# Kernel optimization log

Hardware: AMD Instinct MI355X
Metric: run time of the kernel (lower is better)

## Reference

```python
import jax, jax.numpy as jnp
import numpy as np

N_ATOMS = 3
HIDDEN = 256
N_PAIRS = N_ATOMS * (N_ATOMS - 1) // 2  # 3
BATCH = 500000


def setup_inputs() -> dict:
    key = jax.random.key(0)
    ks = jax.random.split(key, 8)
    s1 = 1.0 / np.sqrt(N_PAIRS)
    s2 = 1.0 / np.sqrt(HIDDEN)
    return {
        "x": jax.random.normal(ks[0], (BATCH, N_ATOMS * 3), dtype=jnp.float32),
        "W1": jax.random.normal(ks[1], (N_PAIRS, HIDDEN), dtype=jnp.float32) * s1,
        "b1": jnp.zeros((HIDDEN,), dtype=jnp.float32),
        "W2": jax.random.normal(ks[2], (HIDDEN, HIDDEN), dtype=jnp.float32) * s2,
        "b2": jnp.zeros((HIDDEN,), dtype=jnp.float32),
        "W3": jax.random.normal(ks[3], (HIDDEN, 3), dtype=jnp.float32) * s2,
        "b3": jnp.zeros((3,), dtype=jnp.float32),
    }


def reference(x, W1, b1, W2, b2, W3, b3):
    # --- pairwise bond lengths (vectorized over batch) ---
    pts = x.reshape(-1, N_ATOMS, 3)                       # [B, n_atoms, 3]
    iu, ju = np.triu_indices(N_ATOMS, 1)                  # static index arrays
    diff = pts[:, iu, :] - pts[:, ju, :]                  # [B, n_pairs, 3]
    r = jnp.sqrt(jnp.sum(diff * diff, axis=-1))           # [B, n_pairs]
    # --- MLP: Dense->relu->Dense->relu->Dense (sizes=[256,256,3]) ---
    h = jax.nn.relu(r @ W1 + b1)                          # [B, 256]
    h = jax.nn.relu(h @ W2 + b2)                          # [B, 256]
    w = h @ W3 + b3                                       # [B, 3] -> (w00, w11, w01)
    # --- analytic eigenvalues of symmetric 2x2 [[w00,w01],[w01,w11]] ---
    # eigh returns ascending order: mean -/+ radius
    m = 0.5 * (w[:, 0] + w[:, 1])
    d = 0.5 * (w[:, 0] - w[:, 1])
    rad = jnp.sqrt(d * d + w[:, 2] * w[:, 2])
    return jnp.stack([m - rad, m + rad], axis=-1)         # [B, 2]
```

## Files before the change

### kernel.cpp

```cpp
#include <hip/hip_runtime.h>
#include <hip/hip_bf16.h>
#include <stdint.h>

typedef __attribute__((ext_vector_type(8))) short short8;
typedef __attribute__((ext_vector_type(4))) float f32x4;

#define NCHUNK 15625
#define NBLK 256
#define NTHR 512
#define NWAVE_TOT (NBLK * 8)

__device__ __forceinline__ unsigned short f2bf(float f) {
    unsigned int u = __float_as_uint(f);
    u = (u + 0x7fffu + ((u >> 16) & 1u)) >> 16;
    return (unsigned short)u;
}

__global__ void prep_kernel(const float* __restrict__ W1, const float* __restrict__ b1,
                            const float* __restrict__ W2, const float* __restrict__ b2,
                            const float* __restrict__ W3,
                            uint4* __restrict__ w2p, float4* __restrict__ w1b1,
                            float4* __restrict__ w3b2) {
    int id = blockIdx.x * 256 + threadIdx.x;
    if (id < 8192) {
        int lane = id & 63;
        int f = id >> 6;
        int s = f >> 4, t = f & 15;
        int g = lane >> 4, c = lane & 15;
        int n = t * 16 + c;
        int kbase = s * 32 + g * 8;
        unsigned int w[4];
#pragma unroll
        for (int jj = 0; jj < 4; ++jj) {
            unsigned int lo = f2bf(W2[(kbase + 2 * jj) * 256 + n]);
            unsigned int hi = f2bf(W2[(kbase + 2 * jj + 1) * 256 + n]);
            w[jj] = lo | (hi << 16);
        }
        w2p[id] = make_uint4(w[0], w[1], w[2], w[3]);
    } else if (id < 8448) {
        int k = id - 8192;
        w1b1[k] = make_float4(W1[k], W1[256 + k], W1[512 + k], b1[k]);
    } else if (id < 8704) {
        int c2 = id - 8448;
        w3b2[c2] = make_float4(W3[c2 * 3 + 0], W3[c2 * 3 + 1], W3[c2 * 3 + 2], b2[c2]);
    }
}

__global__ __launch_bounds__(NTHR, 2) void fused_kernel(
    const float* __restrict__ x, const uint4* __restrict__ w2p,
    const float4* __restrict__ w1b1, const float4* __restrict__ w3b2,
    const float* __restrict__ b3, float* __restrict__ out)
{
    extern __shared__ char smem[];
    const int tid = threadIdx.x;
    const int lane = tid & 63;
    const int g = lane >> 4;
    const int lr = lane & 15;

    {
        uint4* ls = (uint4*)smem;
#pragma unroll
        for (int it = 0; it < 16; ++it) {
            int idx = it * NTHR + tid;
            ls[idx] = w2p[idx];
        }
    }
    __syncthreads();

    const float b30 = b3[0], b31 = b3[1], b32 = b3[2];
    const short8* bfr = (const short8*)smem;
    const int gwave = blockIdx.x * 8 + (tid >> 6);

    for (int chunk = gwave; chunk < NCHUNK; chunk += NWAVE_TOT) {
        const int row0 = chunk * 32;

        float q0[2], q1[2], q2[2];
#pragma unroll
        for (int mt = 0; mt < 2; ++mt) {
            const float* xp = x + (long)(row0 + mt * 16 + lr) * 9;
            float d0 = xp[0] - xp[3], d1 = xp[1] - xp[4], d2 = xp[2] - xp[5];
            float e0 = xp[0] - xp[6], e1 = xp[1] - xp[7], e2 = xp[2] - xp[8];
            float f0 = xp[3] - xp[6], f1 = xp[4] - xp[7], f2 = xp[5] - xp[8];
            q0[mt] = sqrtf(d0 * d0 + d1 * d1 + d2 * d2);
            q1[mt] = sqrtf(e0 * e0 + e1 * e1 + e2 * e2);
            q2[mt] = sqrtf(f0 * f0 + f1 * f1 + f2 * f2);
        }

        f32x4 acc[2][16];
        const f32x4 zz = {0.0f, 0.0f, 0.0f, 0.0f};
#pragma unroll
        for (int t = 0; t < 16; ++t) { acc[0][t] = zz; acc[1][t] = zz; }

#pragma unroll 1
        for (int s = 0; s < 8; ++s) {
            short8 a0v, a1v;
#pragma unroll
            for (int j = 0; j < 8; ++j) {
                float4 wb = w1b1[s * 32 + g * 8 + j];
                float h0 = fmaf(q0[0], wb.x, fmaf(q1[0], wb.y, fmaf(q2[0], wb.z, wb.w)));
                float h1 = fmaf(q0[1], wb.x, fmaf(q1[1], wb.y, fmaf(q2[1], wb.z, wb.w)));
                a0v[j] = (short)f2bf(fmaxf(h0, 0.0f));
                a1v[j] = (short)f2bf(fmaxf(h1, 0.0f));
            }
#pragma unroll
            for (int t = 0; t < 16; ++t) {
                short8 bv = bfr[(s * 16 + t) * 64 + lane];
                acc[0][t] = __builtin_amdgcn_mfma_f32_16x16x32_bf16(a0v, bv, acc[0][t], 0, 0, 0);
                acc[1][t] = __builtin_amdgcn_mfma_f32_16x16x32_bf16(a1v, bv, acc[1][t], 0, 0, 0);
            }
        }

        float p[2][4][3];
#pragma unroll
        for (int mt = 0; mt < 2; ++mt)
#pragma unroll
            for (int r = 0; r < 4; ++r) { p[mt][r][0] = 0.f; p[mt][r][1] = 0.f; p[mt][r][2] = 0.f; }

#pragma unroll
        for (int t = 0; t < 16; ++t) {
            float4 wb = w3b2[t * 16 + lr];
#pragma unroll
            for (int mt = 0; mt < 2; ++mt)
#pragma unroll
                for (int r = 0; r < 4; ++r) {
                    float v = fmaxf(acc[mt][t][r] + wb.w, 0.0f);
                    p[mt][r][0] = fmaf(v, wb.x, p[mt][r][0]);
                    p[mt][r][1] = fmaf(v, wb.y, p[mt][r][1]);
                    p[mt][r][2] = fmaf(v, wb.z, p[mt][r][2]);
                }
        }

#pragma unroll
        for (int mt = 0; mt < 2; ++mt)
#pragma unroll
            for (int r = 0; r < 4; ++r)
#pragma unroll
                for (int m = 0; m < 3; ++m) {
                    float v = p[mt][r][m];
                    v += __shfl_xor(v, 1, 16);
                    v += __shfl_xor(v, 2, 16);
                    v += __shfl_xor(v, 4, 16);
                    v += __shfl_xor(v, 8, 16);
                    p[mt][r][m] = v;
                }

        if (lr == 0) {
#pragma unroll
            for (int mt = 0; mt < 2; ++mt)
#pragma unroll
                for (int r = 0; r < 4; ++r) {
                    float w0 = p[mt][r][0] + b30;
                    float w1v = p[mt][r][1] + b31;
                    float w2v = p[mt][r][2] + b32;
                    float mm = 0.5f * (w0 + w1v);
                    float dd = 0.5f * (w0 - w1v);
                    float rad = sqrtf(fmaf(dd, dd, w2v * w2v));
                    int row = row0 + mt * 16 + g * 4 + r;
                    float2 o = make_float2(mm - rad, mm + rad);
                    *(float2*)(out + (long)row * 2) = o;
                }
        }
    }
}

extern "C" void kernel_launch(void* const* d_in, const int* in_sizes, int n_in,
                              void* d_out, int out_size, void* d_ws, size_t ws_size,
                              hipStream_t stream) {
    const float* x  = (const float*)d_in[0];
    const float* W1 = (const float*)d_in[1];
    const float* b1 = (const float*)d_in[2];
    const float* W2 = (const float*)d_in[3];
    const float* b2 = (const float*)d_in[4];
    const float* W3 = (const float*)d_in[5];
    const float* b3 = (const float*)d_in[6];
    float* out = (float*)d_out;

    char* ws = (char*)d_ws;
    uint4*  w2p  = (uint4*)ws;
    float4* w1b1 = (float4*)(ws + 131072);
    float4* w3b2 = (float4*)(ws + 135168);

    (void)hipFuncSetAttribute((const void*)fused_kernel,
                              hipFuncAttributeMaxDynamicSharedMemorySize, 131072);

    prep_kernel<<<34, 256, 0, stream>>>(W1, b1, W2, b2, W3, w2p, w1b1, w3b2);
    fused_kernel<<<NBLK, NTHR, 131072, stream>>>(x, w2p, w1b1, w3b2, b3, out);
}
```

Measured before the change: 161.7 us.

## Transpose MFMA roles, split W2 between LDS and global, fold b2 into accumulator

```diff
diff --git a/kernel.cpp b/kernel.cpp
--- a/kernel.cpp
+++ b/kernel.cpp
@@ -9,11 +9,19 @@
 #define NBLK 256
 #define NTHR 512
 #define NWAVE_TOT (NBLK * 8)
+#define LDS_T 12
+#define LDS_BYTES (LDS_T * 8 * 64 * 16)
 
 __device__ __forceinline__ unsigned short f2bf(float f) {
     unsigned int u = __float_as_uint(f);
     u = (u + 0x7fffu + ((u >> 16) & 1u)) >> 16;
     return (unsigned short)u;
+}
+
+__device__ __forceinline__ uint32_t cvtpk(float lo, float hi) {
+    uint32_t r;
+    asm("v_cvt_pk_bf16_f32 %0, %1, %2" : "=v"(r) : "v"(lo), "v"(hi));
+    return r;
 }
 
 __global__ void prep_kernel(const float* __restrict__ W1, const float* __restrict__ b1,
@@ -49,7 +57,8 @@
 __global__ __launch_bounds__(NTHR, 2) void fused_kernel(
     const float* __restrict__ x, const uint4* __restrict__ w2p,
     const float4* __restrict__ w1b1, const float4* __restrict__ w3b2,
-    const float* __restrict__ b3, float* __restrict__ out)
+    const float* __restrict__ b2, const float* __restrict__ b3,
+    float* __restrict__ out)
 {
     extern __shared__ char smem[];
     const int tid = threadIdx.x;
@@ -60,15 +69,18 @@
     {
         uint4* ls = (uint4*)smem;
 #pragma unroll
-        for (int it = 0; it < 16; ++it) {
+        for (int it = 0; it < LDS_T; ++it) {
             int idx = it * NTHR + tid;
-            ls[idx] = w2p[idx];
+            int lane2 = idx & 63;
+            int f2 = idx >> 6;
+            int s2 = f2 / LDS_T, t2 = f2 % LDS_T;
+            ls[idx] = w2p[(s2 * 16 + t2) * 64 + lane2];
         }
     }
     __syncthreads();
 
     const float b30 = b3[0], b31 = b3[1], b32 = b3[2];
-    const short8* bfr = (const short8*)smem;
+    const short8* afr = (const short8*)smem;
     const int gwave = blockIdx.x * 8 + (tid >> 6);
 
     for (int chunk = gwave; chunk < NCHUNK; chunk += NWAVE_TOT) {
@@ -76,89 +88,92 @@
 
         float q0[2], q1[2], q2[2];
 #pragma unroll
-        for (int mt = 0; mt < 2; ++mt) {
-            const float* xp = x + (long)(row0 + mt * 16 + lr) * 9;
+        for (int nt = 0; nt < 2; ++nt) {
+            const float* xp = x + (long)(row0 + nt * 16 + lr) * 9;
             float d0 = xp[0] - xp[3], d1 = xp[1] - xp[4], d2 = xp[2] - xp[5];
             float e0 = xp[0] - xp[6], e1 = xp[1] - xp[7], e2 = xp[2] - xp[8];
             float f0 = xp[3] - xp[6], f1 = xp[4] - xp[7], f2 = xp[5] - xp[8];
-            q0[mt] = sqrtf(d0 * d0 + d1 * d1 + d2 * d2);
-            q1[mt] = sqrtf(e0 * e0 + e1 * e1 + e2 * e2);
-            q2[mt] = sqrtf(f0 * f0 + f1 * f1 + f2 * f2);
-        }
-
-        f32x4 acc[2][16];
-        const f32x4 zz = {0.0f, 0.0f, 0.0f, 0.0f};
-#pragma unroll
-        for (int t = 0; t < 16; ++t) { acc[0][t] = zz; acc[1][t] = zz; }
+            q0[nt] = sqrtf(d0 * d0 + d1 * d1 + d2 * d2);
+            q1[nt] = sqrtf(e0 * e0 + e1 * e1 + e2 * e2);
+            q2[nt] = sqrtf(f0 * f0 + f1 * f1 + f2 * f2);
+        }
+
+        f32x4 acc[16][2];
+#pragma unroll
+        for (int t = 0; t < 16; ++t) {
+            float4 bv = *(const float4*)(b2 + t * 16 + g * 4);
+            f32x4 bi; bi[0] = bv.x; bi[1] = bv.y; bi[2] = bv.z; bi[3] = bv.w;
+            acc[t][0] = bi; acc[t][1] = bi;
+        }
 
 #pragma unroll 1
         for (int s = 0; s < 8; ++s) {
-            short8 a0v, a1v;
-#pragma unroll
-            for (int j = 0; j < 8; ++j) {
-                float4 wb = w1b1[s * 32 + g * 8 + j];
-                float h0 = fmaf(q0[0], wb.x, fmaf(q1[0], wb.y, fmaf(q2[0], wb.z, wb.w)));
-                float h1 = fmaf(q0[1], wb.x, fmaf(q1[1], wb.y, fmaf(q2[1], wb.z, wb.w)));
-                a0v[j] = (short)f2bf(fmaxf(h0, 0.0f));
-                a1v[j] = (short)f2bf(fmaxf(h1, 0.0f));
-            }
-#pragma unroll
-            for (int t = 0; t < 16; ++t) {
-                short8 bv = bfr[(s * 16 + t) * 64 + lane];
-                acc[0][t] = __builtin_amdgcn_mfma_f32_16x16x32_bf16(a0v, bv, acc[0][t], 0, 0, 0);
-                acc[1][t] = __builtin_amdgcn_mfma_f32_16x16x32_bf16(a1v, bv, acc[1][t], 0, 0, 0);
-            }
-        }
-
-        float p[2][4][3];
-#pragma unroll
-        for (int mt = 0; mt < 2; ++mt)
-#pragma unroll
-            for (int r = 0; r < 4; ++r) { p[mt][r][0] = 0.f; p[mt][r][1] = 0.f; p[mt][r][2] = 0.f; }
-
+            uint4 fv[4];
+#pragma unroll
+            for (int tv = 0; tv < 4; ++tv)
+                fv[tv] = w2p[(s * 16 + LDS_T + tv) * 64 + lane];
+
+            union { short8 s8; uint32_t u[4]; } pk0, pk1;
+#pragma unroll
+            for (int jj = 0; jj < 4; ++jj) {
+                float4 wa = w1b1[s * 32 + g * 8 + 2 * jj];
+                float4 wb = w1b1[s * 32 + g * 8 + 2 * jj + 1];
+                float h0a = fmaf(q0[0], wa.x, fmaf(q1[0], wa.y, fmaf(q2[0], wa.z, wa.w)));
+                float h0b = fmaf(q0[0], wb.x, fmaf(q1[0], wb.y, fmaf(q2[0], wb.z, wb.w)));
+                float h1a = fmaf(q0[1], wa.x, fmaf(q1[1], wa.y, fmaf(q2[1], wa.z, wa.w)));
+                float h1b = fmaf(q0[1], wb.x, fmaf(q1[1], wb.y, fmaf(q2[1], wb.z, wb.w)));
+                pk0.u[jj] = cvtpk(fmaxf(h0a, 0.0f), fmaxf(h0b, 0.0f));
+                pk1.u[jj] = cvtpk(fmaxf(h1a, 0.0f), fmaxf(h1b, 0.0f));
+            }
+            const short8 bv0 = pk0.s8, bv1 = pk1.s8;
+
+#pragma unroll
+            for (int t = 0; t < LDS_T; ++t) {
+                short8 av = afr[(s * LDS_T + t) * 64 + lane];
+                acc[t][0] = __builtin_amdgcn_mfma_f32_16x16x32_bf16(av, bv0, acc[t][0], 0, 0, 0);
+                acc[t][1] = __builtin_amdgcn_mfma_f32_16x16x32_bf16(av, bv1, acc[t][1], 0, 0, 0);
+            }
+#pragma unroll
+            for (int tv = 0; tv < 4; ++tv) {
+                union { uint4 q; short8 s8; } cvt; cvt.q = fv[tv];
+                acc[LDS_T + tv][0] = __builtin_amdgcn_mfma_f32_16x16x32_bf16(cvt.s8, bv0, acc[LDS_T + tv][0], 0, 0, 0);
+                acc[LDS_T + tv][1] = __builtin_amdgcn_mfma_f32_16x16x32_bf16(cvt.s8, bv1, acc[LDS_T + tv][1], 0, 0, 0);
+            }
+        }
+
+        float p00 = 0.f, p01 = 0.f, p02 = 0.f;
+        float p10 = 0.f, p11 = 0.f, p12 = 0.f;
 #pragma unroll
         for (int t = 0; t < 16; ++t) {
-            float4 wb = w3b2[t * 16 + lr];
-#pragma unroll
-            for (int mt = 0; mt < 2; ++mt)
-#pragma unroll
-                for (int r = 0; r < 4; ++r) {
-                    float v = fmaxf(acc[mt][t][r] + wb.w, 0.0f);
-                    p[mt][r][0] = fmaf(v, wb.x, p[mt][r][0]);
-                    p[mt][r][1] = fmaf(v, wb.y, p[mt][r][1]);
-                    p[mt][r][2] = fmaf(v, wb.z, p[mt][r][2]);
-                }
-        }
-
-#pragma unroll
-        for (int mt = 0; mt < 2; ++mt)
-#pragma unroll
-            for (int r = 0; r < 4; ++r)
-#pragma unroll
-                for (int m = 0; m < 3; ++m) {
-                    float v = p[mt][r][m];
-                    v += __shfl_xor(v, 1, 16);
-                    v += __shfl_xor(v, 2, 16);
-                    v += __shfl_xor(v, 4, 16);
-                    v += __shfl_xor(v, 8, 16);
-                    p[mt][r][m] = v;
-                }
-
-        if (lr == 0) {
-#pragma unroll
-            for (int mt = 0; mt < 2; ++mt)
-#pragma unroll
-                for (int r = 0; r < 4; ++r) {
-                    float w0 = p[mt][r][0] + b30;
-                    float w1v = p[mt][r][1] + b31;
-                    float w2v = p[mt][r][2] + b32;
-                    float mm = 0.5f * (w0 + w1v);
-                    float dd = 0.5f * (w0 - w1v);
-                    float rad = sqrtf(fmaf(dd, dd, w2v * w2v));
-                    int row = row0 + mt * 16 + g * 4 + r;
-                    float2 o = make_float2(mm - rad, mm + rad);
-                    *(float2*)(out + (long)row * 2) = o;
-                }
+#pragma unroll
+            for (int r = 0; r < 4; ++r) {
+                float4 w3 = w3b2[t * 16 + g * 4 + r];
+                float v0 = fmaxf(acc[t][0][r], 0.0f);
+                float v1 = fmaxf(acc[t][1][r], 0.0f);
+                p00 = fmaf(v0, w3.x, p00); p01 = fmaf(v0, w3.y, p01); p02 = fmaf(v0, w3.z, p02);
+                p10 = fmaf(v1, w3.x, p10); p11 = fmaf(v1, w3.y, p11); p12 = fmaf(v1, w3.z, p12);
+            }
+        }
+
+#pragma unroll
+        for (int i = 0; i < 1; ++i) { }
+        p00 += __shfl_xor(p00, 16, 64); p00 += __shfl_xor(p00, 32, 64);
+        p01 += __shfl_xor(p01, 16, 64); p01 += __shfl_xor(p01, 32, 64);
+        p02 += __shfl_xor(p02, 16, 64); p02 += __shfl_xor(p02, 32, 64);
+        p10 += __shfl_xor(p10, 16, 64); p10 += __shfl_xor(p10, 32, 64);
+        p11 += __shfl_xor(p11, 16, 64); p11 += __shfl_xor(p11, 32, 64);
+        p12 += __shfl_xor(p12, 16, 64); p12 += __shfl_xor(p12, 32, 64);
+
+        if (g < 2) {
+            float w0 = (g == 0 ? p00 : p10) + b30;
+            float w1v = (g == 0 ? p01 : p11) + b31;
+            float wc = (g == 0 ? p02 : p12) + b32;
+            float mm = 0.5f * (w0 + w1v);
+            float dd = 0.5f * (w0 - w1v);
+            float rad = sqrtf(fmaf(dd, dd, wc * wc));
+            int row = row0 + g * 16 + lr;
+            float2 o = make_float2(mm - rad, mm + rad);
+            *(float2*)(out + (long)row * 2) = o;
         }
     }
 }
@@ -181,8 +196,8 @@
     float4* w3b2 = (float4*)(ws + 135168);
 
     (void)hipFuncSetAttribute((const void*)fused_kernel,
-                              hipFuncAttributeMaxDynamicSharedMemorySize, 131072);
+                              hipFuncAttributeMaxDynamicSharedMemorySize, LDS_BYTES);
 
     prep_kernel<<<34, 256, 0, stream>>>(W1, b1, W2, b2, W3, w2p, w1b1, w3b2);
-    fused_kernel<<<NBLK, NTHR, 131072, stream>>>(x, w2p, w1b1, w3b2, b3, out);
-}
+    fused_kernel<<<NBLK, NTHR, LDS_BYTES, stream>>>(x, w2p, w1b1, w3b2, b2, b3, out);
+}
```

Result: slower. 179.3 us (+10.9%).
